# Optimization experiments

Hardware: AMD Instinct MI355X
Metric: run time of the kernel (lower is better)

The kernel has to match this reference:

```python
import jax, jax.numpy as jnp
import numpy as np

DT = 0.1
NUM_STEPS = 10
THRESHOLD = 0.3


def setup_inputs() -> dict:
    key = jax.random.key(0)
    k1, k2, k3 = jax.random.split(key, 3)
    B, T, D = 8, 4096, 1024
    L, O = 3, 4
    x = jax.random.normal(k1, (B, T, D), dtype=jnp.float32)
    # nn.Linear(dim, O, bias=False) weights per level, stacked: (L, O, D)
    W = jax.random.normal(k2, (L, O, D), dtype=jnp.float32) / np.sqrt(D)
    # omegas init: randn*0.1 + freq_scales[min(i,2)], freq_scales=[4.0,2.0,0.6]
    freq = jnp.array([4.0, 2.0, 0.6], dtype=jnp.float32)[:, None]
    omegas = jax.random.normal(k3, (L, O), dtype=jnp.float32) * 0.1 + freq
    # coupling strengths: 1.0 + i*0.5
    Ks = 1.0 + 0.5 * jnp.arange(L, dtype=jnp.float32)
    return {"x": x, "W": W, "omegas": omegas, "Ks": Ks}


def reference(x, W, omegas, Ks):
    B, T, D = x.shape
    L, O, _ = W.shape
    two_pi = 2.0 * jnp.pi

    # per-level projection: (L, B, T, O)
    proj = jnp.einsum('btd,lod->lbto', x, W)
    # initial phases from adjacent oscillator ratio
    phases = jnp.arctan2(proj, jnp.roll(proj, 1, axis=-1) + 1e-8) % two_pi

    om = omegas[:, None, None, :]      # (L,1,1,O)
    K = Ks[:, None, None, None]        # (L,1,1,1)

    def step(ph, _):
        # mean phase over time dim per oscillator (circular mean)
        mean_phase = jnp.arctan2(jnp.sin(ph).mean(axis=2, keepdims=True),
                                 jnp.cos(ph).mean(axis=2, keepdims=True))
        coupling = K * jnp.sin(mean_phase - ph) / T
        return (ph + DT * (om + coupling)) % two_pi, None

    phases, _ = jax.lax.scan(step, phases, None, length=NUM_STEPS)

    s = jnp.sin(phases)
    c = jnp.cos(phases)
    # global coherence: |mean_t exp(i*phi)| averaged over oscillators -> (B, L)
    level_coherences = jnp.sqrt(s.mean(axis=2) ** 2 + c.mean(axis=2) ** 2).mean(-1).T

    # sliding window-of-3 coherence along T -> (L, B, T-2)
    ms = (s[:, :, :-2] + s[:, :, 1:-1] + s[:, :, 2:]) / 3.0
    mc = (c[:, :, :-2] + c[:, :, 1:-1] + c[:, :, 2:]) / 3.0
    coh = jnp.sqrt(ms ** 2 + mc ** 2).mean(-1)
    # local-minimum dip detection: boundary at coherence index i+1 (i in 1..T-5)
    cond = (coh[..., 1:-1] < coh[..., :-2] - THRESHOLD) & \
           (coh[..., 1:-1] < coh[..., 2:] - THRESHOLD)      # (L, B, T-4)
    boundary_mask = jnp.pad(cond, ((0, 0), (0, 0), (2, 0)))   # (L, B, T-2)

    return phases, level_coherences, boundary_mask
```

## Files before the change

kernel.cpp:

```cpp
#include <hip/hip_runtime.h>
#include <math.h>

#define NB 8
#define NT 4096
#define ND 1024
#define NL 3
#define NO 4
#define NLO 12
#define NROWS (NB * NT)
#define TWO_PI_D 6.283185307179586476925286766559
#define DT_D 0.1
#define NSTEPS 10
#define THRESH_D 0.3

typedef double f64x4 __attribute__((ext_vector_type(4)));

__global__ __launch_bounds__(256) void k_wprep(const float* __restrict__ W,
                                               double* __restrict__ wsWt)
{
    int i = blockIdx.x * 256 + threadIdx.x;
    if (i < 1024 * 16) {
        int k = i >> 4, col = i & 15;
        wsWt[i] = (col < NLO) ? (double)W[col * ND + k] : 0.0;
    }
}

__global__ __launch_bounds__(512, 6) void k_proj(
    const float* __restrict__ x, const double* __restrict__ wsWt,
    double* __restrict__ ws_proj)
{
    __shared__ char buf[4 * 32 * 68 * 4];
    float*  xs  = reinterpret_cast<float*>(buf);
    double* red = reinterpret_cast<double*>(buf);

    const int tid  = threadIdx.x;
    const int lane = tid & 63;
    const int wid  = tid >> 6;
    const int tile = wid & 1;
    const int kq   = wid >> 1;
    const long row0 = (long)blockIdx.x * 32;

    f64x4 acc = {0.0, 0.0, 0.0, 0.0};

    for (int r = 0; r < 4; ++r) {
        if (r) __syncthreads();
#pragma unroll
        for (int p = 0; p < 4; ++p) {
            int idx = tid + p * 512;
            int w   = idx >> 9;
            int row = (idx >> 4) & 31;
            int sl  = idx & 15;
            float4 v = *reinterpret_cast<const float4*>(
                x + (row0 + row) * ND + w * 256 + r * 64 + sl * 4);
            *reinterpret_cast<float4*>(&xs[(w * 32 + row) * 68 + sl * 4]) = v;
        }
        __syncthreads();

        const float* arow =
            &xs[(kq * 32 + tile * 16 + (lane & 15)) * 68 + (lane >> 4)];
        const double* wb =
            wsWt + (long)(kq * 256 + r * 64 + (lane >> 4)) * 16 + (lane & 15);

        double bv[4], bn[4];
#pragma unroll
        for (int q = 0; q < 4; ++q) bv[q] = wb[q * 64];
#pragma unroll
        for (int g = 0; g < 4; ++g) {
            if (g < 3) {
#pragma unroll
                for (int q = 0; q < 4; ++q) bn[q] = wb[(g * 4 + 4 + q) * 64];
            }
#pragma unroll
            for (int q = 0; q < 4; ++q) {
                double a = (double)arow[(g * 4 + q) * 4];
                acc = __builtin_amdgcn_mfma_f64_16x16x4f64(a, bv[q], acc, 0, 0, 0);
            }
#pragma unroll
            for (int q = 0; q < 4; ++q) bv[q] = bn[q];
        }
    }

    f64x4 z = {0.0, 0.0, 0.0, 0.0};
    f64x4 d1 = __builtin_amdgcn_mfma_f64_16x16x4f64((double)(lane & 15), 1.0, z, 0, 0, 0);
    f64x4 d2 = __builtin_amdgcn_mfma_f64_16x16x4f64(1.0, (double)(lane & 15), z, 0, 0, 0);

    __syncthreads();
#pragma unroll
    for (int n = 0; n < 4; ++n)
        red[(wid * 64 + lane) * 4 + n] = acc[n];
    __syncthreads();
    if (kq == 0) {
#pragma unroll
        for (int n = 0; n < 4; ++n) {
            double v = (red[((0 + tile) * 64 + lane) * 4 + n] +
                        red[((2 + tile) * 64 + lane) * 4 + n]) +
                       (red[((4 + tile) * 64 + lane) * 4 + n] +
                        red[((6 + tile) * 64 + lane) * 4 + n]);
            int i = (int)(d1[n] * 0.25 + 0.5);
            int j = (int)(d2[n] * 0.25 + 0.5);
            if (j < NLO)
                ws_proj[(long)j * NROWS + row0 + tile * 16 + i] = v;
        }
    }
}

#define B_THREADS 512
#define B_ELEMS (NT / B_THREADS)

__global__ __launch_bounds__(B_THREADS) void k_kuramoto(
    const float* __restrict__ omegas, const float* __restrict__ Ks,
    const double* __restrict__ ws_proj, float* __restrict__ ws_s,
    float* __restrict__ ws_c, double* __restrict__ ws_r,
    float* __restrict__ out_ph)
{
    const int g = blockIdx.x;
    const int l = g >> 5;
    const int b = (g >> 2) & 7;
    const int o = g & 3;
    const double om = (double)omegas[l * NO + o];
    const double Kv = (double)Ks[l];
    const double dtom = DT_D * om;
    const double cKT = DT_D * Kv / (double)NT;
    double sA, cA; sincos(dtom, &sA, &cA);
    const int tid = threadIdx.x;
    const int wid = tid >> 6;
    const int lane = tid & 63;
    __shared__ double lds[16];

    const double* pA = ws_proj + (long)(l * NO + o) * NROWS + (long)b * NT;
    const double* pB = ws_proj + (long)(l * NO + ((o + 3) & 3)) * NROWS + (long)b * NT;

    double ph[B_ELEMS], s[B_ELEMS], c[B_ELEMS];
#pragma unroll
    for (int k = 0; k < B_ELEMS; ++k) {
        int t = tid + k * B_THREADS;
        double y = pA[t];
        double xx = pB[t] + 1e-8;
        double p = atan2(y, xx);
        if (p < 0.0) p += TWO_PI_D;
        ph[k] = p;
        double r2 = sqrt(y * y + xx * xx);
        if (r2 > 0.0) { s[k] = y / r2; c[k] = xx / r2; }
        else          { s[k] = 0.0;    c[k] = 1.0; }
    }

    for (int step = 0; step < NSTEPS; ++step) {
        double ts = 0.0, tc = 0.0;
#pragma unroll
        for (int k = 0; k < B_ELEMS; ++k) { ts += s[k]; tc += c[k]; }
#pragma unroll
        for (int off = 32; off > 0; off >>= 1) {
            ts += __shfl_down(ts, off);
            tc += __shfl_down(tc, off);
        }
        if (lane == 0) { lds[wid] = ts; lds[8 + wid] = tc; }
        __syncthreads();
        double S = 0.0, C = 0.0;
#pragma unroll
        for (int w = 0; w < 8; ++w) { S += lds[w]; C += lds[8 + w]; }
        double rr = sqrt(S * S + C * C);
        double sm, cm;
        if (rr > 0.0) { sm = S / rr; cm = C / rr; } else { sm = 0.0; cm = 1.0; }
#pragma unroll
        for (int k = 0; k < B_ELEMS; ++k) {
            double sv = sm * c[k] - cm * s[k];
            double eps = cKT * sv;
            double val = ph[k] + (dtom + eps);
            if (val >= TWO_PI_D) val -= TWO_PI_D;
            if (val < 0.0) val += TWO_PI_D;
            ph[k] = val;
            double sd = fma(cA, eps, sA);
            double cd = fma(-sA, eps, cA);
            double sn = fma(s[k], cd, c[k] * sd);
            double cn = fma(c[k], cd, -(s[k] * sd));
            s[k] = sn; c[k] = cn;
        }
        __syncthreads();
    }
    {
        double ts = 0.0, tc = 0.0;
#pragma unroll
        for (int k = 0; k < B_ELEMS; ++k) { ts += s[k]; tc += c[k]; }
#pragma unroll
        for (int off = 32; off > 0; off >>= 1) {
            ts += __shfl_down(ts, off);
            tc += __shfl_down(tc, off);
        }
        if (lane == 0) { lds[wid] = ts; lds[8 + wid] = tc; }
        __syncthreads();
        if (tid == 0) {
            double S = 0.0, C = 0.0;
#pragma unroll
            for (int w = 0; w < 8; ++w) { S += lds[w]; C += lds[8 + w]; }
            double Sm = S / (double)NT, Cm = C / (double)NT;
            ws_r[g] = sqrt(Sm * Sm + Cm * Cm);
        }
    }
#pragma unroll
    for (int k = 0; k < B_ELEMS; ++k) {
        int t = tid + k * B_THREADS;
        long idx = (long)g * NT + t;
        ws_s[idx] = (float)s[k]; ws_c[idx] = (float)c[k];
        out_ph[((long)(l * NB + b) * NT + t) * NO + o] = (float)ph[k];
    }
}

__global__ __launch_bounds__(256) void k_mask(
    const float* __restrict__ ws_s, const float* __restrict__ ws_c,
    float* __restrict__ out_mask)
{
    const int bid = blockIdx.x;
    const int lb = bid >> 4;
    const int t0 = ((bid & 15) << 8) + threadIdx.x;
    float* mrow = out_mask + (long)lb * (NT - 2);
    if ((bid & 15) == 0 && threadIdx.x < 2) mrow[threadIdx.x] = 0.0f;
    if (t0 >= NT - 4) return;
    double q[3] = {0.0, 0.0, 0.0};
#pragma unroll
    for (int o = 0; o < NO; ++o) {
        const float* ps = ws_s + ((long)lb * NO + o) * NT + t0;
        const float* pc = ws_c + ((long)lb * NO + o) * NT + t0;
        double sv[5], cv[5];
#pragma unroll
        for (int j = 0; j < 5; ++j) { sv[j] = (double)ps[j]; cv[j] = (double)pc[j]; }
#pragma unroll
        for (int j = 0; j < 3; ++j) {
            double ms = ((sv[j] + sv[j + 1]) + sv[j + 2]) / 3.0;
            double mc = ((cv[j] + cv[j + 1]) + cv[j + 2]) / 3.0;
            q[j] += sqrt(ms * ms + mc * mc);
        }
    }
    double coh0 = q[0] / 4.0, coh1 = q[1] / 4.0, coh2 = q[2] / 4.0;
    bool cond = (coh1 < coh0 - THRESH_D) && (coh1 < coh2 - THRESH_D);
    mrow[2 + t0] = cond ? 1.0f : 0.0f;
}

__global__ void k_level(const double* __restrict__ ws_r, float* __restrict__ out_lvl)
{
    const int tid = threadIdx.x;
    if (tid < NB * NL) {
        const int b = tid / NL, l = tid % NL;
        const double* r = ws_r + (long)(l * NB + b) * NO;
        double m = (((r[0] + r[1]) + r[2]) + r[3]) / 4.0;
        out_lvl[tid] = (float)m;
    }
}

extern "C" void kernel_launch(void* const* d_in, const int* in_sizes, int n_in,
                              void* d_out, int out_size, void* d_ws, size_t ws_size,
                              hipStream_t stream)
{
    const float* x      = (const float*)d_in[0];
    const float* W      = (const float*)d_in[1];
    const float* omegas = (const float*)d_in[2];
    const float* Ks     = (const float*)d_in[3];
    float* out = (float*)d_out;

    double* wsWt    = (double*)d_ws;
    double* ws_proj = wsWt + 1024 * 16;
    float*  ws_s    = (float*)(ws_proj + (long)NLO * NROWS);
    float*  ws_c    = ws_s + (long)NLO * NB * NT;
    double* ws_r    = (double*)(ws_c + (long)NLO * NB * NT);

    float* out_ph   = out;
    float* out_lvl  = out + 393216;
    float* out_mask = out + 393240;

    k_wprep<<<64, 256, 0, stream>>>(W, wsWt);
    k_proj<<<NROWS / 32, 512, 0, stream>>>(x, wsWt, ws_proj);
    k_kuramoto<<<NL * NB * NO, B_THREADS, 0, stream>>>(omegas, Ks, ws_proj, ws_s, ws_c, ws_r, out_ph);
    k_mask<<<24 * 16, 256, 0, stream>>>(ws_s, ws_c, out_mask);
    k_level<<<1, 64, 0, stream>>>(ws_r, out_lvl);
}
```

Baseline: 70.31 us.

## Restructure projection GEMM to per-wave K-slices with 4 row tiles and register prefetch

The projection kernel moves from 32-row blocks of 512 threads, which staged a shared tile behind block-wide barriers, to 64-row blocks of 256 threads. Each wave owns a 256-wide K slice and a private LDS tile, and it accumulates four 16-row MFMA tiles so each B fragment loaded from global is reused four times. The next x slice is prefetched into registers while the current one is computed, so the main loop no longer needs block barriers. In exchange, each thread holds more accumulator registers, and writes to the per-wave LDS tile rely on lockstep execution within the wave rather than explicit synchronisation.

```diff
diff --git a/kernel.cpp b/kernel.cpp
--- a/kernel.cpp
+++ b/kernel.cpp
@@ -25,58 +25,65 @@
     }
 }
 
-__global__ __launch_bounds__(512, 6) void k_proj(
+__global__ __launch_bounds__(256) void k_proj(
     const float* __restrict__ x, const double* __restrict__ wsWt,
     double* __restrict__ ws_proj)
 {
-    __shared__ char buf[4 * 32 * 68 * 4];
-    float*  xs  = reinterpret_cast<float*>(buf);
-    double* red = reinterpret_cast<double*>(buf);
+    __shared__ double red[4 * 4 * 64 * 4];
+    float* xl = reinterpret_cast<float*>(red);
 
     const int tid  = threadIdx.x;
     const int lane = tid & 63;
     const int wid  = tid >> 6;
-    const int tile = wid & 1;
-    const int kq   = wid >> 1;
-    const long row0 = (long)blockIdx.x * 32;
-
-    f64x4 acc = {0.0, 0.0, 0.0, 0.0};
-
-    for (int r = 0; r < 4; ++r) {
-        if (r) __syncthreads();
+    const int m    = lane & 15;
+    const int kk   = lane >> 4;
+    const long row0 = (long)blockIdx.x * 64;
+
+    float* wtile = xl + wid * 1280;
+    const float* xg = x + row0 * ND + wid * 256;
+
+    f64x4 acc[4];
+#pragma unroll
+    for (int t = 0; t < 4; ++t) acc[t] = (f64x4){0.0, 0.0, 0.0, 0.0};
+
+    {
+        float4 fr[4];
+#pragma unroll
+        for (int p = 0; p < 4; ++p)
+            fr[p] = *reinterpret_cast<const float4*>(
+                xg + (long)(m + 16 * p) * ND + kk * 4);
+#pragma unroll
+        for (int p = 0; p < 4; ++p)
+            *reinterpret_cast<float4*>(
+                &wtile[(m + 16 * p) * 20 + kk * 4]) = fr[p];
+    }
+
+#pragma unroll 1
+    for (int ss = 0; ss < 16; ++ss) {
+        float4 fr[4];
+        if (ss < 15) {
+#pragma unroll
+            for (int p = 0; p < 4; ++p)
+                fr[p] = *reinterpret_cast<const float4*>(
+                    xg + (long)(m + 16 * p) * ND + 16 * (ss + 1) + kk * 4);
+        }
+        double bv[4];
+#pragma unroll
+        for (int p = 0; p < 4; ++p)
+            bv[p] = wsWt[(long)(wid * 256 + 16 * ss + 4 * p + kk) * 16 + m];
 #pragma unroll
         for (int p = 0; p < 4; ++p) {
-            int idx = tid + p * 512;
-            int w   = idx >> 9;
-            int row = (idx >> 4) & 31;
-            int sl  = idx & 15;
-            float4 v = *reinterpret_cast<const float4*>(
-                x + (row0 + row) * ND + w * 256 + r * 64 + sl * 4);
-            *reinterpret_cast<float4*>(&xs[(w * 32 + row) * 68 + sl * 4]) = v;
-        }
-        __syncthreads();
-
-        const float* arow =
-            &xs[(kq * 32 + tile * 16 + (lane & 15)) * 68 + (lane >> 4)];
-        const double* wb =
-            wsWt + (long)(kq * 256 + r * 64 + (lane >> 4)) * 16 + (lane & 15);
-
-        double bv[4], bn[4];
-#pragma unroll
-        for (int q = 0; q < 4; ++q) bv[q] = wb[q * 64];
-#pragma unroll
-        for (int g = 0; g < 4; ++g) {
-            if (g < 3) {
-#pragma unroll
-                for (int q = 0; q < 4; ++q) bn[q] = wb[(g * 4 + 4 + q) * 64];
+#pragma unroll
+            for (int t = 0; t < 4; ++t) {
+                double a = (double)wtile[(t * 16 + m) * 20 + 4 * p + kk];
+                acc[t] = __builtin_amdgcn_mfma_f64_16x16x4f64(a, bv[p], acc[t], 0, 0, 0);
             }
-#pragma unroll
-            for (int q = 0; q < 4; ++q) {
-                double a = (double)arow[(g * 4 + q) * 4];
-                acc = __builtin_amdgcn_mfma_f64_16x16x4f64(a, bv[q], acc, 0, 0, 0);
-            }
-#pragma unroll
-            for (int q = 0; q < 4; ++q) bv[q] = bn[q];
+        }
+        if (ss < 15) {
+#pragma unroll
+            for (int p = 0; p < 4; ++p)
+                *reinterpret_cast<float4*>(
+                    &wtile[(m + 16 * p) * 20 + kk * 4]) = fr[p];
         }
     }
 
@@ -86,21 +93,22 @@
 
     __syncthreads();
 #pragma unroll
-    for (int n = 0; n < 4; ++n)
-        red[(wid * 64 + lane) * 4 + n] = acc[n];
+    for (int t = 0; t < 4; ++t)
+#pragma unroll
+        for (int n = 0; n < 4; ++n)
+            red[((wid * 4 + t) * 64 + lane) * 4 + n] = acc[t][n];
     __syncthreads();
-    if (kq == 0) {
-#pragma unroll
-        for (int n = 0; n < 4; ++n) {
-            double v = (red[((0 + tile) * 64 + lane) * 4 + n] +
-                        red[((2 + tile) * 64 + lane) * 4 + n]) +
-                       (red[((4 + tile) * 64 + lane) * 4 + n] +
-                        red[((6 + tile) * 64 + lane) * 4 + n]);
-            int i = (int)(d1[n] * 0.25 + 0.5);
-            int j = (int)(d2[n] * 0.25 + 0.5);
-            if (j < NLO)
-                ws_proj[(long)j * NROWS + row0 + tile * 16 + i] = v;
-        }
+
+#pragma unroll
+    for (int n = 0; n < 4; ++n) {
+        double v = (red[((0 * 4 + wid) * 64 + lane) * 4 + n] +
+                    red[((1 * 4 + wid) * 64 + lane) * 4 + n]) +
+                   (red[((2 * 4 + wid) * 64 + lane) * 4 + n] +
+                    red[((3 * 4 + wid) * 64 + lane) * 4 + n]);
+        int i = (int)(d1[n] * 0.25 + 0.5);
+        int j = (int)(d2[n] * 0.25 + 0.5);
+        if (j < NLO)
+            ws_proj[(long)j * NROWS + row0 + wid * 16 + i] = v;
     }
 }
 
@@ -267,7 +275,7 @@
     float* out_mask = out + 393240;
 
     k_wprep<<<64, 256, 0, stream>>>(W, wsWt);
-    k_proj<<<NROWS / 32, 512, 0, stream>>>(x, wsWt, ws_proj);
+    k_proj<<<NROWS / 64, 256, 0, stream>>>(x, wsWt, ws_proj);
     k_kuramoto<<<NL * NB * NO, B_THREADS, 0, stream>>>(omegas, Ks, ws_proj, ws_s, ws_c, ws_r, out_ph);
     k_mask<<<24 * 16, 256, 0, stream>>>(ws_s, ws_c, out_mask);
     k_level<<<1, 64, 0, stream>>>(ws_r, out_lvl);
```

Measured after the change: 95.82 us. 36.3% more time.
